# Performance work log

Measured on AMD Instinct MI355X. Metric: run time of the kernel, lower is better.

The kernel has to match this reference:

```python
import jax, jax.numpy as jnp
import numpy as np

B, F, H, A, P, E = 65536, 512, 256, 4, 2, 32


def _mlp2(x, W1, b1, W2, b2):
    # two stacked Linear layers (no activation, matching the torch module)
    return (x @ W1 + b1) @ W2 + b2


def setup_inputs() -> dict:
    key = jax.random.key(0)
    ks = iter(jax.random.split(key, 32))
    s = 0.02  # small init scale, mimics orthogonal(gain=0.01)/renormed init
    d = {
        "features": jax.random.normal(next(ks), (B, F), jnp.float32),
        "pointgoal": jax.random.normal(next(ks), (B, P), jnp.float32),
        "a0_W1": s * jax.random.normal(next(ks), (F, H), jnp.float32),
        "a0_b1": jnp.zeros((H,), jnp.float32),
        "a0_W2": s * jax.random.normal(next(ks), (H, A), jnp.float32),
        "a0_b2": jnp.zeros((A,), jnp.float32),
        "a1_W1": s * jax.random.normal(next(ks), (F, H), jnp.float32),
        "a1_b1": jnp.zeros((H,), jnp.float32),
        "a1_W2": s * jax.random.normal(next(ks), (H, A), jnp.float32),
        "a1_b2": jnp.zeros((A,), jnp.float32),
        "a2_Wp": s * jax.random.normal(next(ks), (P, E), jnp.float32),
        "a2_bp": jnp.zeros((E,), jnp.float32),
        "a2_W1": s * jax.random.normal(next(ks), (F + E, H), jnp.float32),
        "a2_b1": jnp.zeros((H,), jnp.float32),
        "a2_W2": s * jax.random.normal(next(ks), (H, A), jnp.float32),
        "a2_b2": jnp.zeros((A,), jnp.float32),
        "c0_W1": s * jax.random.normal(next(ks), (F, H), jnp.float32),
        "c0_b1": jnp.zeros((H,), jnp.float32),
        "c0_W2": s * jax.random.normal(next(ks), (H, 1), jnp.float32),
        "c0_b2": jnp.zeros((1,), jnp.float32),
        "c1_W1": s * jax.random.normal(next(ks), (F, H), jnp.float32),
        "c1_b1": jnp.zeros((H,), jnp.float32),
        "c1_W2": s * jax.random.normal(next(ks), (H, 1), jnp.float32),
        "c1_b2": jnp.zeros((1,), jnp.float32),
        "c2_Wp": s * jax.random.normal(next(ks), (P, E), jnp.float32),
        "c2_bp": jnp.zeros((E,), jnp.float32),
        "c2_W1": s * jax.random.normal(next(ks), (F + E, H), jnp.float32),
        "c2_b1": jnp.zeros((H,), jnp.float32),
        "c2_W2": s * jax.random.normal(next(ks), (H, 1), jnp.float32),
        "c2_b2": jnp.zeros((1,), jnp.float32),
        "task_id": jax.random.randint(next(ks), (B, 1), 0, 3, jnp.int32),
    }
    return d


def reference(features, pointgoal,
              a0_W1, a0_b1, a0_W2, a0_b2,
              a1_W1, a1_b1, a1_W2, a1_b2,
              a2_Wp, a2_bp, a2_W1, a2_b1, a2_W2, a2_b2,
              c0_W1, c0_b1, c0_W2, c0_b2,
              c1_W1, c1_b1, c1_W2, c1_b2,
              c2_Wp, c2_bp, c2_W1, c2_b1, c2_W2, c2_b2,
              task_id):
    # obs-conditioned heads: embed pointgoal and concat with features
    xa2 = jnp.concatenate([features, pointgoal @ a2_Wp + a2_bp], axis=1)
    xc2 = jnp.concatenate([features, pointgoal @ c2_Wp + c2_bp], axis=1)

    logits0 = _mlp2(features, a0_W1, a0_b1, a0_W2, a0_b2)   # [B, A]
    logits1 = _mlp2(features, a1_W1, a1_b1, a1_W2, a1_b2)
    logits2 = _mlp2(xa2,      a2_W1, a2_b1, a2_W2, a2_b2)

    value0 = _mlp2(features, c0_W1, c0_b1, c0_W2, c0_b2)    # [B, 1]
    value1 = _mlp2(features, c1_W1, c1_b1, c1_W2, c1_b2)
    value2 = _mlp2(xc2,      c2_W1, c2_b1, c2_W2, c2_b2)

    # group-concat + argsort recombination == per-sample select by task_id
    tid = task_id  # [B, 1]
    logits = jnp.where(tid == 0, logits0, jnp.where(tid == 1, logits1, logits2))
    value = jnp.where(tid == 0, value0, jnp.where(tid == 1, value1, value2))
    return jnp.concatenate([value, logits], axis=1)  # [B, 1 + A]
```

## Files before the change

kernel.cpp:

```cpp
#include <hip/hip_runtime.h>
#include <stdint.h>


typedef __attribute__((ext_vector_type(8))) short bf16x8;
typedef __attribute__((ext_vector_type(4))) float f32x4;

__device__ __forceinline__ unsigned short f2bf(float f) {
    union { unsigned int i; float f; } v; v.f = f;
    unsigned int u = v.i;
    return (unsigned short)((u + 0x7fffu + ((u >> 16) & 1u)) >> 16);
}
__device__ __forceinline__ unsigned int pkbf(float a, float b) {
    union { unsigned int i; float f; } va, vb; va.f = a; vb.f = b;
    unsigned int ua = (va.i + 0x7fffu + ((va.i >> 16) & 1u)) >> 16;
    unsigned int ub = (vb.i + 0x7fffu + ((vb.i >> 16) & 1u)) & 0xffff0000u;
    return (ua & 0xffffu) | ub;
}

struct HeadPtrs {
    const float* W1[6];
    const float* b1[6];
    const float* W2[6];
    const float* b2[6];
};

__global__ void precompute_main(HeadPtrs hp, float* __restrict__ Mfull) {
    int c = blockIdx.x;
    int tid = threadIdx.x;
    int k = blockIdx.y * 256 + tid;
    int hd, a;
    if (c == 0)       { hd = 3; a = 0; }
    else if (c < 5)   { hd = 0; a = c - 1; }
    else if (c == 5)  { hd = 4; a = 0; }
    else if (c < 10)  { hd = 1; a = c - 6; }
    else if (c == 10) { hd = 5; a = 0; }
    else              { hd = 2; a = c - 11; }
    int Kh = (hd == 2 || hd == 5) ? 544 : 512;
    int A  = (hd < 3) ? 4 : 1;

    __shared__ float w2s[256];
    w2s[tid] = hp.W2[hd][tid * A + a];
    __syncthreads();
    if (k > Kh) return;

    const float* row = (k < Kh) ? (hp.W1[hd] + (size_t)k * 256) : hp.b1[hd];
    float acc = (k == Kh) ? hp.b2[hd][a] : 0.f;
    const float4* r4 = (const float4*)row;
    #pragma unroll 8
    for (int j0 = 0; j0 < 64; ++j0) {
        float4 w = r4[j0];
        acc += w.x * w2s[j0 * 4]     + w.y * w2s[j0 * 4 + 1]
             + w.z * w2s[j0 * 4 + 2] + w.w * w2s[j0 * 4 + 3];
    }
    Mfull[c * 548 + k] = acc;
}

__global__ void precompute_pack(const float* __restrict__ Mfull,
                                const float* __restrict__ a2Wp,
                                const float* __restrict__ a2bp,
                                const float* __restrict__ c2Wp,
                                const float* __restrict__ c2bp,
                                uint4* __restrict__ bfrag,
                                float* __restrict__ bias,
                                float* __restrict__ V) {
    int idx = blockIdx.x * 256 + threadIdx.x;
    int s = idx >> 6, l = idx & 63;
    int q = l >> 4, c = l & 15;
    unsigned int w[4];
    #pragma unroll
    for (int jj = 0; jj < 4; ++jj) {
        int k0 = s * 32 + q * 8 + 2 * jj;
        unsigned short lo = (c < 15) ? f2bf(Mfull[c * 548 + k0])     : (unsigned short)0;
        unsigned short hi = (c < 15) ? f2bf(Mfull[c * 548 + k0 + 1]) : (unsigned short)0;
        w[jj] = (unsigned int)lo | ((unsigned int)hi << 16);
    }
    bfrag[idx] = make_uint4(w[0], w[1], w[2], w[3]);

    if (blockIdx.x == 0 && threadIdx.x < 16) {
        int cc = threadIdx.x;
        float b = 0.f, v0 = 0.f, v1 = 0.f;
        if (cc < 15) {
            int Kh = (cc >= 10) ? 544 : 512;
            b = Mfull[cc * 548 + Kh];
            if (cc >= 10) {
                const float* Wp = (cc == 10) ? c2Wp : a2Wp;
                const float* bp = (cc == 10) ? c2bp : a2bp;
                #pragma unroll 8
                for (int e = 0; e < 32; ++e) {
                    float t = Mfull[cc * 548 + 512 + e];
                    b  += bp[e] * t;
                    v0 += Wp[e] * t;
                    v1 += Wp[32 + e] * t;
                }
            }
        }
        bias[cc] = b; V[cc] = v0; V[16 + cc] = v1;
    }
}

__global__ __launch_bounds__(256) void main_gemm(
    const float* __restrict__ feat,
    const float* __restrict__ pg,
    const int* __restrict__ task,
    const uint4* __restrict__ bfrag,
    const float* __restrict__ bias,
    const float* __restrict__ V,
    float* __restrict__ out)
{
    __shared__ uint4 lds_b[1024];
    int tid = threadIdx.x;
    #pragma unroll
    for (int i = 0; i < 4; ++i) lds_b[tid + 256 * i] = bfrag[tid + 256 * i];
    __syncthreads();

    int l = tid & 63;
    int tile = blockIdx.x * 4 + (tid >> 6);
    int row0 = tile * 16;
    int m = l & 15, q = l >> 4;

    const float4* f4 = (const float4*)feat;
    size_t abase = (size_t)(row0 + m) * 128 + q * 2;

    f32x4 acc = {0.f, 0.f, 0.f, 0.f};
    #pragma unroll
    for (int s = 0; s < 16; ++s) {
        float4 x0 = f4[abase + s * 8];
        float4 x1 = f4[abase + s * 8 + 1];
        uint4 av;
        av.x = pkbf(x0.x, x0.y);
        av.y = pkbf(x0.z, x0.w);
        av.z = pkbf(x1.x, x1.y);
        av.w = pkbf(x1.z, x1.w);
        uint4 bv = lds_b[s * 64 + l];
        acc = __builtin_amdgcn_mfma_f32_16x16x32_bf16(
            __builtin_bit_cast(bf16x8, av), __builtin_bit_cast(bf16x8, bv),
            acc, 0, 0, 0);
    }

    int c = m;
    int tc = c / 5;
    int jc = c - 5 * tc;
    float bc = bias[c], v0 = V[c], v1 = V[16 + c];
    const float2* pg2 = (const float2*)pg;
    #pragma unroll
    for (int i = 0; i < 4; ++i) {
        int r = row0 + q * 4 + i;
        float2 p = pg2[r];
        float val = acc[i] + bc + p.x * v0 + p.y * v1;
        if (c < 15 && task[r] == tc) out[(size_t)r * 5 + jc] = val;
    }
}

extern "C" void kernel_launch(void* const* d_in, const int* in_sizes, int n_in,
                              void* d_out, int out_size, void* d_ws, size_t ws_size,
                              hipStream_t stream)
{
    const float* feat = (const float*)d_in[0];
    const float* pg   = (const float*)d_in[1];
    const int w1_idx[6] = {2, 6, 12, 16, 20, 26};
    HeadPtrs hp;
    for (int h = 0; h < 6; ++h) {
        hp.W1[h] = (const float*)d_in[w1_idx[h]];
        hp.b1[h] = (const float*)d_in[w1_idx[h] + 1];
        hp.W2[h] = (const float*)d_in[w1_idx[h] + 2];
        hp.b2[h] = (const float*)d_in[w1_idx[h] + 3];
    }
    const float* a2Wp = (const float*)d_in[10];
    const float* a2bp = (const float*)d_in[11];
    const float* c2Wp = (const float*)d_in[24];
    const float* c2bp = (const float*)d_in[25];
    const int* task = (const int*)d_in[30];
    float* out = (float*)d_out;
    int B = in_sizes[0] / 512;

    char* ws = (char*)d_ws;
    float* Mfull = (float*)ws;
    uint4* bfrag = (uint4*)(ws + 32896);
    float* bias  = (float*)(ws + 32896 + 16384);
    float* V     = (float*)(ws + 32896 + 16384 + 64);

    precompute_main<<<dim3(15, 3), 256, 0, stream>>>(hp, Mfull);
    precompute_pack<<<dim3(4), 256, 0, stream>>>(Mfull, a2Wp, a2bp, c2Wp, c2bp,
                                                 bfrag, bias, V);
    int tiles = B / 16;
    main_gemm<<<dim3(tiles / 4), 256, 0, stream>>>(feat, pg, task, bfrag, bias, V, out);
}
```

Baseline: 262.5 us.

## Fuse precompute kernels and batch feature loads in main GEMM

Merges the two precompute kernels into one, so each thread writes its bf16 fragment directly and the last y-block computes bias and pointgoal terms from shared memory. This removes one launch and the intermediate Mfull buffer. The main GEMM now issues its feature loads in two batches of eight iterations, overlapping the second batch with the first batch's MFMAs, and adds a launch_bounds occupancy hint. The batched loads raise register pressure.

```diff
diff --git a/kernel.cpp b/kernel.cpp
--- a/kernel.cpp
+++ b/kernel.cpp
@@ -24,10 +24,18 @@
     const float* b2[6];
 };
 
-__global__ void precompute_main(HeadPtrs hp, float* __restrict__ Mfull) {
+__global__ void precompute(HeadPtrs hp,
+                           const float* __restrict__ a2Wp,
+                           const float* __restrict__ a2bp,
+                           const float* __restrict__ c2Wp,
+                           const float* __restrict__ c2bp,
+                           unsigned short* __restrict__ bfrag_u,
+                           float* __restrict__ bias,
+                           float* __restrict__ V) {
     int c = blockIdx.x;
+    int y = blockIdx.y;
     int tid = threadIdx.x;
-    int k = blockIdx.y * 256 + tid;
+    int k = y * 256 + tid;
     int hd, a;
     if (c == 0)       { hd = 3; a = 0; }
     else if (c < 5)   { hd = 0; a = c - 1; }
@@ -39,66 +47,54 @@
     int A  = (hd < 3) ? 4 : 1;
 
     __shared__ float w2s[256];
+    __shared__ float tail[40];
     w2s[tid] = hp.W2[hd][tid * A + a];
     __syncthreads();
-    if (k > Kh) return;
-
-    const float* row = (k < Kh) ? (hp.W1[hd] + (size_t)k * 256) : hp.b1[hd];
-    float acc = (k == Kh) ? hp.b2[hd][a] : 0.f;
-    const float4* r4 = (const float4*)row;
-    #pragma unroll 8
-    for (int j0 = 0; j0 < 64; ++j0) {
-        float4 w = r4[j0];
-        acc += w.x * w2s[j0 * 4]     + w.y * w2s[j0 * 4 + 1]
-             + w.z * w2s[j0 * 4 + 2] + w.w * w2s[j0 * 4 + 3];
-    }
-    Mfull[c * 548 + k] = acc;
-}
-
-__global__ void precompute_pack(const float* __restrict__ Mfull,
-                                const float* __restrict__ a2Wp,
-                                const float* __restrict__ a2bp,
-                                const float* __restrict__ c2Wp,
-                                const float* __restrict__ c2bp,
-                                uint4* __restrict__ bfrag,
-                                float* __restrict__ bias,
-                                float* __restrict__ V) {
-    int idx = blockIdx.x * 256 + threadIdx.x;
-    int s = idx >> 6, l = idx & 63;
-    int q = l >> 4, c = l & 15;
-    unsigned int w[4];
-    #pragma unroll
-    for (int jj = 0; jj < 4; ++jj) {
-        int k0 = s * 32 + q * 8 + 2 * jj;
-        unsigned short lo = (c < 15) ? f2bf(Mfull[c * 548 + k0])     : (unsigned short)0;
-        unsigned short hi = (c < 15) ? f2bf(Mfull[c * 548 + k0 + 1]) : (unsigned short)0;
-        w[jj] = (unsigned int)lo | ((unsigned int)hi << 16);
-    }
-    bfrag[idx] = make_uint4(w[0], w[1], w[2], w[3]);
-
-    if (blockIdx.x == 0 && threadIdx.x < 16) {
-        int cc = threadIdx.x;
-        float b = 0.f, v0 = 0.f, v1 = 0.f;
-        if (cc < 15) {
-            int Kh = (cc >= 10) ? 544 : 512;
-            b = Mfull[cc * 548 + Kh];
-            if (cc >= 10) {
-                const float* Wp = (cc == 10) ? c2Wp : a2Wp;
-                const float* bp = (cc == 10) ? c2bp : a2bp;
+
+    float acc = 0.f;
+    if (k <= Kh) {
+        const float* row = (k < Kh) ? (hp.W1[hd] + (size_t)k * 256) : hp.b1[hd];
+        acc = (k == Kh) ? hp.b2[hd][a] : 0.f;
+        const float4* r4 = (const float4*)row;
+        #pragma unroll 8
+        for (int j0 = 0; j0 < 64; ++j0) {
+            float4 w = r4[j0];
+            acc += w.x * w2s[j0 * 4]     + w.y * w2s[j0 * 4 + 1]
+                 + w.z * w2s[j0 * 4 + 2] + w.w * w2s[j0 * 4 + 3];
+        }
+    }
+
+    if (y < 2) {
+        int s = k >> 5, q = (k >> 3) & 3, j = k & 7;
+        bfrag_u[((s * 64 + q * 16 + c) * 8) + j] = f2bf(acc);
+        if (c == 0)
+            bfrag_u[((s * 64 + q * 16 + 15) * 8) + j] = 0;
+    } else {
+        if (k <= Kh) tail[k - 512] = acc;
+        __syncthreads();
+        if (tid == 0) {
+            float b, v0 = 0.f, v1 = 0.f;
+            if (Kh == 512) {
+                b = tail[0];
+            } else {
+                b = tail[32];
+                const float* Wp = (c == 10) ? c2Wp : a2Wp;
+                const float* bp = (c == 10) ? c2bp : a2bp;
                 #pragma unroll 8
                 for (int e = 0; e < 32; ++e) {
-                    float t = Mfull[cc * 548 + 512 + e];
+                    float t = tail[e];
                     b  += bp[e] * t;
                     v0 += Wp[e] * t;
                     v1 += Wp[32 + e] * t;
                 }
             }
+            bias[c] = b; V[c] = v0; V[16 + c] = v1;
         }
-        bias[cc] = b; V[cc] = v0; V[16 + cc] = v1;
-    }
-}
-
-__global__ __launch_bounds__(256) void main_gemm(
+        if (c == 0 && tid == 1) { bias[15] = 0.f; V[15] = 0.f; V[31] = 0.f; }
+    }
+}
+
+__global__ __launch_bounds__(256, 4) void main_gemm(
     const float* __restrict__ feat,
     const float* __restrict__ pg,
     const int* __restrict__ task,
@@ -121,19 +117,36 @@
     const float4* f4 = (const float4*)feat;
     size_t abase = (size_t)(row0 + m) * 128 + q * 2;
 
+    float4 L[8], M[8];
+    uint4 av[8];
     f32x4 acc = {0.f, 0.f, 0.f, 0.f};
-    #pragma unroll
-    for (int s = 0; s < 16; ++s) {
-        float4 x0 = f4[abase + s * 8];
-        float4 x1 = f4[abase + s * 8 + 1];
-        uint4 av;
-        av.x = pkbf(x0.x, x0.y);
-        av.y = pkbf(x0.z, x0.w);
-        av.z = pkbf(x1.x, x1.y);
-        av.w = pkbf(x1.z, x1.w);
+
+    #pragma unroll
+    for (int s = 0; s < 8; ++s) { L[s] = f4[abase + s * 8]; M[s] = f4[abase + s * 8 + 1]; }
+    #pragma unroll
+    for (int s = 0; s < 8; ++s) {
+        av[s].x = pkbf(L[s].x, L[s].y); av[s].y = pkbf(L[s].z, L[s].w);
+        av[s].z = pkbf(M[s].x, M[s].y); av[s].w = pkbf(M[s].z, M[s].w);
+    }
+    #pragma unroll
+    for (int s = 0; s < 8; ++s) { L[s] = f4[abase + (s + 8) * 8]; M[s] = f4[abase + (s + 8) * 8 + 1]; }
+    #pragma unroll
+    for (int s = 0; s < 8; ++s) {
         uint4 bv = lds_b[s * 64 + l];
         acc = __builtin_amdgcn_mfma_f32_16x16x32_bf16(
-            __builtin_bit_cast(bf16x8, av), __builtin_bit_cast(bf16x8, bv),
+            __builtin_bit_cast(bf16x8, av[s]), __builtin_bit_cast(bf16x8, bv),
+            acc, 0, 0, 0);
+    }
+    #pragma unroll
+    for (int s = 0; s < 8; ++s) {
+        av[s].x = pkbf(L[s].x, L[s].y); av[s].y = pkbf(L[s].z, L[s].w);
+        av[s].z = pkbf(M[s].x, M[s].y); av[s].w = pkbf(M[s].z, M[s].w);
+    }
+    #pragma unroll
+    for (int s = 0; s < 8; ++s) {
+        uint4 bv = lds_b[(s + 8) * 64 + l];
+        acc = __builtin_amdgcn_mfma_f32_16x16x32_bf16(
+            __builtin_bit_cast(bf16x8, av[s]), __builtin_bit_cast(bf16x8, bv),
             acc, 0, 0, 0);
     }
 
@@ -174,14 +187,14 @@
     int B = in_sizes[0] / 512;
 
     char* ws = (char*)d_ws;
-    float* Mfull = (float*)ws;
-    uint4* bfrag = (uint4*)(ws + 32896);
-    float* bias  = (float*)(ws + 32896 + 16384);
-    float* V     = (float*)(ws + 32896 + 16384 + 64);
-
-    precompute_main<<<dim3(15, 3), 256, 0, stream>>>(hp, Mfull);
-    precompute_pack<<<dim3(4), 256, 0, stream>>>(Mfull, a2Wp, a2bp, c2Wp, c2bp,
-                                                 bfrag, bias, V);
+    unsigned short* bfrag_u = (unsigned short*)ws;
+    float* bias  = (float*)(ws + 16384);
+    float* V     = (float*)(ws + 16384 + 64);
+
+    precompute<<<dim3(15, 3), 256, 0, stream>>>(hp, a2Wp, a2bp, c2Wp, c2bp,
+                                                bfrag_u, bias, V);
     int tiles = B / 16;
-    main_gemm<<<dim3(tiles / 4), 256, 0, stream>>>(feat, pg, task, bfrag, bias, V, out);
-}
+    main_gemm<<<dim3(tiles / 4), 256, 0, stream>>>(feat, pg, task,
+                                                   (const uint4*)bfrag_u,
+                                                   bias, V, out);
+}
```

New measurement: 258.0 us. About the same (-1.7%).
